# Optimization experiments

Measured on AMD Instinct MI355X. Metric: run time of the kernel, lower is better.

Reference implementation:

```python
import jax, jax.numpy as jnp
import numpy as np
import math

D_MODEL = 1024
N_HEADS = 16
DH = D_MODEL // N_HEADS
THETA = 10000.0


def _rope_tables(S):
    # freqs: (dh/2,)
    inv_freq = 1.0 / (THETA ** (jnp.arange(0, DH, 2, dtype=jnp.float32) / DH))
    ang = jnp.arange(S, dtype=jnp.float32)[:, None] * inv_freq[None, :]  # (S, dh/2)
    cos = jnp.concatenate([jnp.cos(ang), jnp.cos(ang)], axis=-1)  # (S, dh)
    sin = jnp.concatenate([jnp.sin(ang), jnp.sin(ang)], axis=-1)
    return cos, sin


def _apply_rope(x, cos, sin):
    # x: (B, S, H, dh); rotate-half RoPE
    x1, x2 = jnp.split(x, 2, axis=-1)
    rot = jnp.concatenate([-x2, x1], axis=-1)
    c = cos[None, :, None, :]
    s = sin[None, :, None, :]
    return x * c + rot * s


def setup_inputs() -> dict:
    key = jax.random.key(0)
    k1, k2, k3 = jax.random.split(key, 3)
    x = jax.random.normal(k1, (4, 2048, D_MODEL), dtype=jnp.float32)
    qkv = 0.01 * jax.random.normal(k2, (3 * D_MODEL, D_MODEL), dtype=jnp.float32)
    wo = 0.01 * jax.random.normal(k3, (D_MODEL, D_MODEL), dtype=jnp.float32)
    return {"x": x, "qkv": qkv, "wo": wo}


def reference(x, qkv, wo):
    B, S, D = x.shape
    QKV = x @ qkv.T  # (B, S, 3D)
    Q, K, V = jnp.split(QKV, 3, axis=-1)
    q = Q.reshape(B, S, N_HEADS, DH)
    k = K.reshape(B, S, N_HEADS, DH)
    v = V.reshape(B, S, N_HEADS, DH)
    cos, sin = _rope_tables(S)
    q = _apply_rope(q, cos, sin)
    k = _apply_rope(k, cos, sin)
    # (B, H, S, dh)
    q = q.transpose(0, 2, 1, 3)
    k = k.transpose(0, 2, 1, 3)
    v = v.transpose(0, 2, 1, 3)
    scores = jnp.einsum("bhsd,bhtd->bhst", q, k) / math.sqrt(float(DH))
    mask = jnp.tril(jnp.ones((S, S), dtype=scores.dtype))
    scores = scores * mask
    # faithful to original: any exact-zero entry (masked or incidental) -> -inf
    scores = jnp.where(scores == 0.0, -jnp.inf, scores)
    attn = jax.nn.softmax(scores, axis=-1)
    out = jnp.einsum("bhst,bhtd->bhsd", attn, v)  # (B, H, S, dh)
    out = out.transpose(0, 2, 1, 3).reshape(B, S, D)
    return out @ wo.T
```

## Files before the change

kernel.cpp:

```cpp
#include <hip/hip_runtime.h>
#include <math.h>

typedef __bf16 bf16x8 __attribute__((ext_vector_type(8)));
typedef __bf16 bf16x4 __attribute__((ext_vector_type(4)));
typedef float  floatx4 __attribute__((ext_vector_type(4)));
typedef float  floatx2 __attribute__((ext_vector_type(2)));

#define AS1(p) ((__attribute__((address_space(1))) void*)(p))
#define AS3(p) ((__attribute__((address_space(3))) void*)(p))

#define MASKV (-1.0e30f)
#define SOFTMAX_SCALE_LOG2 0.1803368801111244f
#define ROPE_LOG2F 0.4152410118609203f

#define BARRIER do { __builtin_amdgcn_sched_barrier(0); \
                     __builtin_amdgcn_s_barrier(); \
                     __builtin_amdgcn_sched_barrier(0); } while (0)

__global__ __launch_bounds__(256)
void cvt3_kernel(const float* __restrict__ x, const float* __restrict__ qkv,
                 const float* __restrict__ wo, __bf16* __restrict__ xb,
                 __bf16* __restrict__ qkvb, __bf16* __restrict__ wob,
                 float* __restrict__ rt)
{
    const int bi = blockIdx.x;
    if (bi >= 12288) {
        const int e0 = (bi - 12288) * 1024 + threadIdx.x * 4;
#pragma unroll
        for (int j = 0; j < 4; ++j) {
            const int e = e0 + j;
            const int s = e >> 5, d = e & 31;
            const float f = exp2f(-(float)d * ROPE_LOG2F);
            float sn, cs;
            sincosf((float)s * f, &sn, &cs);
            floatx2 t; t[0] = cs; t[1] = sn;
            *(floatx2*)(rt + e * 2) = t;
        }
        return;
    }
    const float* src;
    __bf16* dst;
    int base;
    if (bi < 8192)       { src = x;   dst = xb;   base = bi * 1024; }
    else if (bi < 11264) { src = qkv; dst = qkvb; base = (bi - 8192) * 1024; }
    else                 { src = wo;  dst = wob;  base = (bi - 11264) * 1024; }

    const int i = base + threadIdx.x * 4;
    const floatx4 v = *(const floatx4*)(src + i);
    bf16x4 o;
    o[0] = (__bf16)v[0]; o[1] = (__bf16)v[1];
    o[2] = (__bf16)v[2]; o[3] = (__bf16)v[3];
    *(bf16x4*)(dst + i) = o;
}

__device__ __forceinline__ void gemm_pipe(const __bf16* __restrict__ Ap,
                                          const __bf16* __restrict__ Bp,
                                          const int m0, const int n0,
                                          __bf16* smem, floatx4 (&acc)[4][4])
{
    const int tid  = threadIdx.x;
    const int wave = tid >> 6;
    const int lane = tid & 63;
    const int quad = lane >> 4;
    const int l16  = lane & 15;
    const int wr   = wave >> 2;
    const int wc   = wave & 3;

    const int arow = wr * 32 + l16;
    const int brow = (wc & 1) * 64 + l16;
    const int bsel = (wc >> 1) * 8192;
    const int swz  = (l16 & 7) << 4;
    int coff[2];
    coff[0] = (( (quad << 4))        ^ swz) >> 1;
    coff[1] = ((64 | (quad << 4))    ^ swz) >> 1;

    auto stageA = [&](int buf, int h, int k0) {
        const int o = tid << 4;
        const int r = o >> 7;
        const int c = (o & 127) ^ ((r & 7) << 4);
        const __bf16* src = Ap + (size_t)(m0 + h * 64 + r) * 1024 + k0 + (c >> 1);
        __builtin_amdgcn_global_load_lds(AS1(src),
            AS3(smem + buf * 24576 + h * 4096 + wave * 512), 16, 0, 0);
    };
    auto stageB = [&](int buf, int h, int k0) {
#pragma unroll
        for (int q = 0; q < 2; ++q) {
            const int o = (q * 512 + tid) << 4;
            const int r = o >> 7;
            const int c = (o & 127) ^ ((r & 7) << 4);
            const __bf16* src = Bp + (size_t)(n0 + h * 128 + r) * 1024 + k0 + (c >> 1);
            __builtin_amdgcn_global_load_lds(AS1(src),
                AS3(smem + buf * 24576 + 8192 + h * 8192 + (q * 8 + wave) * 512), 16, 0, 0);
        }
    };

#define RDA(P, qm, fm, ks) (*(const bf16x8*)(smem + (P) * 24576 + (qm) * 4096 \
                             + ((arow + (fm) * 16) << 6) + coff[ks]))
#define RDB(P, g, ks)      (*(const bf16x8*)(smem + (P) * 24576 + 8192 + bsel \
                             + ((brow + (g) * 16) << 6) + coff[ks]))
#define MFMA8(MB, NB, AV, BV) do { \
    _Pragma("unroll") for (int fm_ = 0; fm_ < 2; ++fm_) \
    _Pragma("unroll") for (int gi_ = 0; gi_ < 2; ++gi_) \
    _Pragma("unroll") for (int ks_ = 0; ks_ < 2; ++ks_) \
        acc[(MB) + fm_][(NB) + gi_] = __builtin_amdgcn_mfma_f32_16x16x32_bf16( \
            AV[fm_][ks_], BV[gi_][ks_], acc[(MB) + fm_][(NB) + gi_], 0, 0, 0); \
} while (0)

    stageA(0, 0, 0);  stageB(0, 0, 0);  stageA(0, 1, 0);  stageB(0, 1, 0);
    stageA(1, 0, 64); stageB(1, 0, 64); stageA(1, 1, 64);
    asm volatile("s_waitcnt vmcnt(4)" ::: "memory");
    BARRIER;

    bf16x8 a0[2][2], a1[2][2], b0[2][2], b1[2][2];

#define TILE(JT, P) do { \
    const int kn_ = ((JT) + 2) * 64; \
     \
    _Pragma("unroll") for (int f_ = 0; f_ < 2; ++f_) \
    _Pragma("unroll") for (int k_ = 0; k_ < 2; ++k_) a0[f_][k_] = RDA(P, 0, f_, k_); \
    _Pragma("unroll") for (int g_ = 0; g_ < 2; ++g_) \
    _Pragma("unroll") for (int k_ = 0; k_ < 2; ++k_) b0[g_][k_] = RDB(P, g_, k_); \
    if ((JT) + 1 < 16) stageB(1 - (P), 1, ((JT) + 1) * 64); \
    BARRIER; \
    __builtin_amdgcn_s_setprio(1); MFMA8(0, 0, a0, b0); __builtin_amdgcn_s_setprio(0); \
    BARRIER; \
     \
    _Pragma("unroll") for (int g_ = 0; g_ < 2; ++g_) \
    _Pragma("unroll") for (int k_ = 0; k_ < 2; ++k_) b1[g_][k_] = RDB(P, 2 + g_, k_); \
    if ((JT) + 2 < 16) stageA(P, 0, kn_); \
    BARRIER; \
    __builtin_amdgcn_s_setprio(1); MFMA8(0, 2, a0, b1); __builtin_amdgcn_s_setprio(0); \
    BARRIER; \
     \
    _Pragma("unroll") for (int f_ = 0; f_ < 2; ++f_) \
    _Pragma("unroll") for (int k_ = 0; k_ < 2; ++k_) a1[f_][k_] = RDA(P, 1, f_, k_); \
    if ((JT) + 2 < 16) stageB(P, 0, kn_); \
    BARRIER; \
    __builtin_amdgcn_s_setprio(1); MFMA8(2, 2, a1, b1); __builtin_amdgcn_s_setprio(0); \
    BARRIER; \
     \
    if ((JT) + 2 < 16) stageA(P, 1, kn_); \
    BARRIER; \
    __builtin_amdgcn_s_setprio(1); MFMA8(2, 0, a1, b0); __builtin_amdgcn_s_setprio(0); \
     \
    if ((JT) + 2 < 16)      { asm volatile("s_waitcnt vmcnt(4)" ::: "memory"); } \
    else if ((JT) + 1 < 16) { asm volatile("s_waitcnt vmcnt(0)" ::: "memory"); } \
    BARRIER; \
} while (0)

    for (int it = 0; it < 8; ++it) {
        TILE(2 * it, 0);
        TILE(2 * it + 1, 1);
    }
#undef TILE
#undef RDA
#undef RDB
#undef MFMA8
}

__global__ __launch_bounds__(512, 2)
void gemm_rope_kernel(const __bf16* __restrict__ A, const __bf16* __restrict__ BT,
                      __bf16* __restrict__ Qr, __bf16* __restrict__ Kr,
                      __bf16* __restrict__ Vt, const float* __restrict__ rt)
{
    extern __shared__ __align__(16) __bf16 smem[];
    const int id  = blockIdx.x;
    const int xcd = id & 7, lid = id >> 3;
    const int tm  = xcd * 8 + lid / 12;
    const int tn  = lid % 12;
    const int m0  = tm * 128, n0 = tn * 256;

    floatx4 acc[4][4] = {};
    gemm_pipe(A, BT, m0, n0, smem, acc);

    const int tid  = threadIdx.x;
    const int wave = tid >> 6;
    const int lane = tid & 63;
    const int quad = lane >> 4, l16 = lane & 15;
    const int wr   = wave >> 2, wc = wave & 3;

    const int gn0    = n0 + wc * 64;
    const int region = gn0 >> 10;
    const int h      = (gn0 >> 6) & 15;

    if (region == 2) {
#pragma unroll
        for (int f = 0; f < 4; ++f) {
            const int gm = m0 + (f >> 1) * 64 + wr * 32 + (f & 1) * 16 + quad * 4;
            const int b = gm >> 11, s = gm & 2047;
#pragma unroll
            for (int g = 0; g < 4; ++g) {
                const int d = g * 16 + l16;
                bf16x4 w;
#pragma unroll
                for (int r = 0; r < 4; ++r) w[r] = (__bf16)acc[f][g][r];
                *(bf16x4*)(Vt + ((size_t)(b * 16 + h) * 64 + d) * 2048 + s) = w;
            }
        }
    } else {
        __bf16* dst = region ? Kr : Qr;
#pragma unroll
        for (int g = 0; g < 2; ++g) {
            const int d1 = g * 16 + l16;
#pragma unroll
            for (int f = 0; f < 4; ++f) {
                const int gm0 = m0 + (f >> 1) * 64 + wr * 32 + (f & 1) * 16 + quad * 4;
                const int b = gm0 >> 11, s0 = gm0 & 2047;
#pragma unroll
                for (int r = 0; r < 4; ++r) {
                    const floatx2 t = *(const floatx2*)(rt + ((s0 + r) * 32 + d1) * 2);
                    const float a1 = acc[f][g][r];
                    const float a2 = acc[f][g + 2][r];
                    __bf16* row = dst + ((size_t)((b * 16 + h) * 2048 + s0 + r)) * 64;
                    row[d1]      = (__bf16)(a1 * t[0] - a2 * t[1]);
                    row[d1 + 32] = (__bf16)(a2 * t[0] + a1 * t[1]);
                }
            }
        }
    }
}

__global__ __launch_bounds__(512, 2)
void gemm_bt_kernel(const __bf16* __restrict__ A, const __bf16* __restrict__ BT,
                    float* __restrict__ C)
{
    extern __shared__ __align__(16) __bf16 smem[];
    const int id  = blockIdx.x;
    const int xcd = id & 7, lid = id >> 3;
    const int tm  = xcd * 8 + (lid >> 2);
    const int tn  = lid & 3;
    const int m0  = tm * 128, n0 = tn * 256;

    floatx4 acc[4][4] = {};
    gemm_pipe(A, BT, m0, n0, smem, acc);

    const int tid  = threadIdx.x;
    const int wave = tid >> 6, lane = tid & 63;
    const int quad = lane >> 4, l16 = lane & 15;
    const int wr   = wave >> 2, wc = wave & 3;

#pragma unroll
    for (int f = 0; f < 4; ++f) {
        const int row = m0 + (f >> 1) * 64 + wr * 32 + (f & 1) * 16 + quad * 4;
#pragma unroll
        for (int g = 0; g < 4; ++g) {
            const int col = n0 + wc * 64 + g * 16 + l16;
#pragma unroll
            for (int r = 0; r < 4; ++r)
                C[(size_t)(row + r) * 1024 + col] = acc[f][g][r];
        }
    }
}

__global__ __launch_bounds__(256, 4)
void attn_kernel(const __bf16* __restrict__ Qr, const __bf16* __restrict__ Kr,
                 const __bf16* __restrict__ Vt, __bf16* __restrict__ ctx)
{
    __shared__ __align__(16) __bf16 Ks[64 * 64];
    __shared__ __align__(16) __bf16 Vs[64 * 64];
    __shared__ __align__(16) __bf16 plds[4][16 * 72];

    const int bh   = blockIdx.x;
    const int b    = bh >> 4, h = bh & 15;
    const int tid  = threadIdx.x;
    const int wave = tid >> 6;
    const int lane = tid & 63;
    const int quad = lane >> 4, l16 = lane & 15;
    const int sw   = l16 & 7;

    const __bf16* Qb = Qr + (size_t)bh * 2048 * 64;
    const __bf16* Kb = Kr + (size_t)bh * 2048 * 64;
    const __bf16* Vb = Vt + (size_t)bh * 64 * 2048;
    __bf16* Pw = &plds[wave][0];

    const int c0   = tid;
    const int row0 = c0 >> 3, jg0 = (c0 & 7) ^ (row0 & 7);
    const int c1   = 256 + tid;
    const int row1 = c1 >> 3, jg1 = (c1 & 7) ^ (row1 & 7);

    const int tiles[2] = { (int)blockIdx.y, 31 - (int)blockIdx.y };

    for (int pass = 0; pass < 2; ++pass) {
        const int q0b  = tiles[pass] * 64;
        const int q0   = q0b + wave * 16;
        const int qa   = q0 + l16;
        const int kend = q0b + 64;

        bf16x8 bq[2];
#pragma unroll
        for (int t = 0; t < 2; ++t)
            bq[t] = *(const bf16x8*)(Qb + (q0 + l16) * 64 + t * 32 + quad * 8);

        floatx4 o[4] = {};
        float lpart = 0.f;

        for (int kt = 0; kt < kend; kt += 64) {
            __builtin_amdgcn_global_load_lds(AS1(Kb + (size_t)(kt + row0) * 64 + jg0 * 8),
                                             AS3(Ks + wave * 512), 16, 0, 0);
            __builtin_amdgcn_global_load_lds(AS1(Vb + (size_t)row0 * 2048 + kt + jg0 * 8),
                                             AS3(Vs + wave * 512), 16, 0, 0);
            __builtin_amdgcn_global_load_lds(AS1(Kb + (size_t)(kt + row1) * 64 + jg1 * 8),
                                             AS3(Ks + (4 + wave) * 512), 16, 0, 0);
            __builtin_amdgcn_global_load_lds(AS1(Vb + (size_t)row1 * 2048 + kt + jg1 * 8),
                                             AS3(Vs + (4 + wave) * 512), 16, 0, 0);
            asm volatile("s_waitcnt vmcnt(0)" ::: "memory");
            __syncthreads();

            floatx4 s[4] = {};
#pragma unroll
            for (int st = 0; st < 4; ++st) {
                bf16x8 ka0 = *(const bf16x8*)(Ks + (st * 16 + l16) * 64 + ((0 + quad) ^ sw) * 8);
                bf16x8 ka1 = *(const bf16x8*)(Ks + (st * 16 + l16) * 64 + ((4 + quad) ^ sw) * 8);
                s[st] = __builtin_amdgcn_mfma_f32_16x16x32_bf16(ka0, bq[0], s[st], 0, 0, 0);
                s[st] = __builtin_amdgcn_mfma_f32_16x16x32_bf16(ka1, bq[1], s[st], 0, 0, 0);
            }

#pragma unroll
            for (int st = 0; st < 4; ++st) {
                bf16x4 w;
#pragma unroll
                for (int r = 0; r < 4; ++r) {
                    const int key = kt + st * 16 + quad * 4 + r;
                    const float v = (key > qa) ? MASKV : s[st][r] * SOFTMAX_SCALE_LOG2;
                    const float p = __builtin_amdgcn_exp2f(v);
                    lpart += p;
                    w[r] = (__bf16)p;
                }
                *(bf16x4*)(Pw + l16 * 72 + st * 16 + quad * 4) = w;
            }

            asm volatile("s_waitcnt lgkmcnt(0)" ::: "memory");
            bf16x8 ap0 = *(const bf16x8*)(Pw + l16 * 72 + quad * 8);
            bf16x8 ap1 = *(const bf16x8*)(Pw + l16 * 72 + 32 + quad * 8);

#pragma unroll
            for (int nt = 0; nt < 4; ++nt) {
                bf16x8 bv0 = *(const bf16x8*)(Vs + (nt * 16 + l16) * 64 + ((0 + quad) ^ sw) * 8);
                bf16x8 bv1 = *(const bf16x8*)(Vs + (nt * 16 + l16) * 64 + ((4 + quad) ^ sw) * 8);
                o[nt] = __builtin_amdgcn_mfma_f32_16x16x32_bf16(ap0, bv0, o[nt], 0, 0, 0);
                o[nt] = __builtin_amdgcn_mfma_f32_16x16x32_bf16(ap1, bv1, o[nt], 0, 0, 0);
            }

            __syncthreads();
        }

        float l = lpart;
        l += __shfl_xor(l, 16, 64);
        l += __shfl_xor(l, 32, 64);
        float lr[4];
#pragma unroll
        for (int r = 0; r < 4; ++r)
            lr[r] = __shfl(l, quad * 4 + r, 64);
#pragma unroll
        for (int nt = 0; nt < 4; ++nt)
#pragma unroll
            for (int r = 0; r < 4; ++r) {
                const int srow = q0 + quad * 4 + r;
                const float inv_l = 1.0f / fmaxf(lr[r], 1e-20f);
                ctx[((size_t)(b * 2048 + srow)) * 1024 + h * 64 + nt * 16 + l16] =
                    (__bf16)(o[nt][r] * inv_l);
            }
    }
}

extern "C" void kernel_launch(void* const* d_in, const int* in_sizes, int n_in,
                              void* d_out, int out_size, void* d_ws, size_t ws_size,
                              hipStream_t stream)
{
    const float* x   = (const float*)d_in[0];
    const float* qkv = (const float*)d_in[1];
    const float* wo  = (const float*)d_in[2];
    float* out = (float*)d_out;

    char* ws = (char*)d_ws;
    const size_t MB = 1024 * 1024;
    __bf16* xb   = (__bf16*)(ws);
    __bf16* qkvb = (__bf16*)(ws + 16 * MB);
    __bf16* wob  = (__bf16*)(ws + 22 * MB);
    __bf16* Qr   = (__bf16*)(ws + 24 * MB);
    __bf16* Kr   = (__bf16*)(ws + 40 * MB);
    __bf16* Vt   = (__bf16*)(ws + 56 * MB);
    __bf16* ctx  = (__bf16*)(ws + 72 * MB);
    float*  rt   = (float*) (ws + 88 * MB);

    hipFuncSetAttribute((const void*)gemm_rope_kernel,
                        hipFuncAttributeMaxDynamicSharedMemorySize, 98304);
    hipFuncSetAttribute((const void*)gemm_bt_kernel,
                        hipFuncAttributeMaxDynamicSharedMemorySize, 98304);

    cvt3_kernel<<<12352, 256, 0, stream>>>(x, qkv, wo, xb, qkvb, wob, rt);
    gemm_rope_kernel<<<768, 512, 98304, stream>>>(xb, qkvb, Qr, Kr, Vt, rt);
    attn_kernel<<<dim3(64, 16), 256, 0, stream>>>(Qr, Kr, Vt, ctx);
    gemm_bt_kernel<<<256, 512, 98304, stream>>>(ctx, wob, out);
}
```

Before: 229.8 us.

## Double-buffer K/V tiles in attention and fold softmax scale into Q

```diff
diff --git a/kernel.cpp b/kernel.cpp
--- a/kernel.cpp
+++ b/kernel.cpp
@@ -115,7 +115,6 @@
 
 #define TILE(JT, P) do { \
     const int kn_ = ((JT) + 2) * 64; \
-     \
     _Pragma("unroll") for (int f_ = 0; f_ < 2; ++f_) \
     _Pragma("unroll") for (int k_ = 0; k_ < 2; ++k_) a0[f_][k_] = RDA(P, 0, f_, k_); \
     _Pragma("unroll") for (int g_ = 0; g_ < 2; ++g_) \
@@ -124,25 +123,21 @@
     BARRIER; \
     __builtin_amdgcn_s_setprio(1); MFMA8(0, 0, a0, b0); __builtin_amdgcn_s_setprio(0); \
     BARRIER; \
-     \
     _Pragma("unroll") for (int g_ = 0; g_ < 2; ++g_) \
     _Pragma("unroll") for (int k_ = 0; k_ < 2; ++k_) b1[g_][k_] = RDB(P, 2 + g_, k_); \
     if ((JT) + 2 < 16) stageA(P, 0, kn_); \
     BARRIER; \
     __builtin_amdgcn_s_setprio(1); MFMA8(0, 2, a0, b1); __builtin_amdgcn_s_setprio(0); \
     BARRIER; \
-     \
     _Pragma("unroll") for (int f_ = 0; f_ < 2; ++f_) \
     _Pragma("unroll") for (int k_ = 0; k_ < 2; ++k_) a1[f_][k_] = RDA(P, 1, f_, k_); \
     if ((JT) + 2 < 16) stageB(P, 0, kn_); \
     BARRIER; \
     __builtin_amdgcn_s_setprio(1); MFMA8(2, 2, a1, b1); __builtin_amdgcn_s_setprio(0); \
     BARRIER; \
-     \
     if ((JT) + 2 < 16) stageA(P, 1, kn_); \
     BARRIER; \
     __builtin_amdgcn_s_setprio(1); MFMA8(2, 0, a1, b0); __builtin_amdgcn_s_setprio(0); \
-     \
     if ((JT) + 2 < 16)      { asm volatile("s_waitcnt vmcnt(4)" ::: "memory"); } \
     else if ((JT) + 1 < 16) { asm volatile("s_waitcnt vmcnt(0)" ::: "memory"); } \
     BARRIER; \
@@ -199,6 +194,7 @@
         }
     } else {
         __bf16* dst = region ? Kr : Qr;
+        const float sc = region ? 1.0f : SOFTMAX_SCALE_LOG2;
 #pragma unroll
         for (int g = 0; g < 2; ++g) {
             const int d1 = g * 16 + l16;
@@ -212,8 +208,8 @@
                     const float a1 = acc[f][g][r];
                     const float a2 = acc[f][g + 2][r];
                     __bf16* row = dst + ((size_t)((b * 16 + h) * 2048 + s0 + r)) * 64;
-                    row[d1]      = (__bf16)(a1 * t[0] - a2 * t[1]);
-                    row[d1 + 32] = (__bf16)(a2 * t[0] + a1 * t[1]);
+                    row[d1]      = (__bf16)((a1 * t[0] - a2 * t[1]) * sc);
+                    row[d1 + 32] = (__bf16)((a2 * t[0] + a1 * t[1]) * sc);
                 }
             }
         }
@@ -252,12 +248,12 @@
     }
 }
 
-__global__ __launch_bounds__(256, 4)
+__global__ __launch_bounds__(256, 3)
 void attn_kernel(const __bf16* __restrict__ Qr, const __bf16* __restrict__ Kr,
                  const __bf16* __restrict__ Vt, __bf16* __restrict__ ctx)
 {
-    __shared__ __align__(16) __bf16 Ks[64 * 64];
-    __shared__ __align__(16) __bf16 Vs[64 * 64];
+    __shared__ __align__(16) __bf16 Ks[2][64 * 64];
+    __shared__ __align__(16) __bf16 Vs[2][64 * 64];
     __shared__ __align__(16) __bf16 plds[4][16 * 72];
 
     const int bh   = blockIdx.x;
@@ -280,11 +276,22 @@
 
     const int tiles[2] = { (int)blockIdx.y, 31 - (int)blockIdx.y };
 
+    auto stage = [&](int buf, int kt) {
+        __builtin_amdgcn_global_load_lds(AS1(Kb + (size_t)(kt + row0) * 64 + jg0 * 8),
+                                         AS3(&Ks[buf][0] + wave * 512), 16, 0, 0);
+        __builtin_amdgcn_global_load_lds(AS1(Vb + (size_t)row0 * 2048 + kt + jg0 * 8),
+                                         AS3(&Vs[buf][0] + wave * 512), 16, 0, 0);
+        __builtin_amdgcn_global_load_lds(AS1(Kb + (size_t)(kt + row1) * 64 + jg1 * 8),
+                                         AS3(&Ks[buf][0] + (4 + wave) * 512), 16, 0, 0);
+        __builtin_amdgcn_global_load_lds(AS1(Vb + (size_t)row1 * 2048 + kt + jg1 * 8),
+                                         AS3(&Vs[buf][0] + (4 + wave) * 512), 16, 0, 0);
+    };
+
     for (int pass = 0; pass < 2; ++pass) {
-        const int q0b  = tiles[pass] * 64;
-        const int q0   = q0b + wave * 16;
-        const int qa   = q0 + l16;
-        const int kend = q0b + 64;
+        const int q0b   = tiles[pass] * 64;
+        const int q0    = q0b + wave * 16;
+        const int qa    = q0 + l16;
+        const int ntile = tiles[pass] + 1;
 
         bf16x8 bq[2];
 #pragma unroll
@@ -294,55 +301,56 @@
         floatx4 o[4] = {};
         float lpart = 0.f;
 
-        for (int kt = 0; kt < kend; kt += 64) {
-            __builtin_amdgcn_global_load_lds(AS1(Kb + (size_t)(kt + row0) * 64 + jg0 * 8),
-                                             AS3(Ks + wave * 512), 16, 0, 0);
-            __builtin_amdgcn_global_load_lds(AS1(Vb + (size_t)row0 * 2048 + kt + jg0 * 8),
-                                             AS3(Vs + wave * 512), 16, 0, 0);
-            __builtin_amdgcn_global_load_lds(AS1(Kb + (size_t)(kt + row1) * 64 + jg1 * 8),
-                                             AS3(Ks + (4 + wave) * 512), 16, 0, 0);
-            __builtin_amdgcn_global_load_lds(AS1(Vb + (size_t)row1 * 2048 + kt + jg1 * 8),
-                                             AS3(Vs + (4 + wave) * 512), 16, 0, 0);
-            asm volatile("s_waitcnt vmcnt(0)" ::: "memory");
-            __syncthreads();
-
-            floatx4 s[4] = {};
-#pragma unroll
-            for (int st = 0; st < 4; ++st) {
-                bf16x8 ka0 = *(const bf16x8*)(Ks + (st * 16 + l16) * 64 + ((0 + quad) ^ sw) * 8);
-                bf16x8 ka1 = *(const bf16x8*)(Ks + (st * 16 + l16) * 64 + ((4 + quad) ^ sw) * 8);
-                s[st] = __builtin_amdgcn_mfma_f32_16x16x32_bf16(ka0, bq[0], s[st], 0, 0, 0);
-                s[st] = __builtin_amdgcn_mfma_f32_16x16x32_bf16(ka1, bq[1], s[st], 0, 0, 0);
-            }
-
-#pragma unroll
-            for (int st = 0; st < 4; ++st) {
-                bf16x4 w;
-#pragma unroll
-                for (int r = 0; r < 4; ++r) {
-                    const int key = kt + st * 16 + quad * 4 + r;
-                    const float v = (key > qa) ? MASKV : s[st][r] * SOFTMAX_SCALE_LOG2;
-                    const float p = __builtin_amdgcn_exp2f(v);
-                    lpart += p;
-                    w[r] = (__bf16)p;
-                }
-                *(bf16x4*)(Pw + l16 * 72 + st * 16 + quad * 4) = w;
-            }
-
-            asm volatile("s_waitcnt lgkmcnt(0)" ::: "memory");
-            bf16x8 ap0 = *(const bf16x8*)(Pw + l16 * 72 + quad * 8);
-            bf16x8 ap1 = *(const bf16x8*)(Pw + l16 * 72 + 32 + quad * 8);
-
-#pragma unroll
-            for (int nt = 0; nt < 4; ++nt) {
-                bf16x8 bv0 = *(const bf16x8*)(Vs + (nt * 16 + l16) * 64 + ((0 + quad) ^ sw) * 8);
-                bf16x8 bv1 = *(const bf16x8*)(Vs + (nt * 16 + l16) * 64 + ((4 + quad) ^ sw) * 8);
-                o[nt] = __builtin_amdgcn_mfma_f32_16x16x32_bf16(ap0, bv0, o[nt], 0, 0, 0);
-                o[nt] = __builtin_amdgcn_mfma_f32_16x16x32_bf16(ap1, bv1, o[nt], 0, 0, 0);
-            }
-
-            __syncthreads();
-        }
+        __syncthreads();
+        stage(0, 0);
+
+#define ATT_TILE(CUR, KT, MASKED, HASNEXT) do {                                   \
+    asm volatile("s_waitcnt vmcnt(0)" ::: "memory");                              \
+    BARRIER;                                                                      \
+    const __bf16* Kc = &Ks[CUR][0];                                               \
+    const __bf16* Vc = &Vs[CUR][0];                                               \
+    floatx4 s[4] = {};                                                            \
+    __builtin_amdgcn_s_setprio(1);                                                \
+    _Pragma("unroll") for (int st = 0; st < 4; ++st) {                            \
+        bf16x8 ka0 = *(const bf16x8*)(Kc + (st * 16 + l16) * 64 + ((0 + quad) ^ sw) * 8); \
+        bf16x8 ka1 = *(const bf16x8*)(Kc + (st * 16 + l16) * 64 + ((4 + quad) ^ sw) * 8); \
+        s[st] = __builtin_amdgcn_mfma_f32_16x16x32_bf16(ka0, bq[0], s[st], 0, 0, 0); \
+        s[st] = __builtin_amdgcn_mfma_f32_16x16x32_bf16(ka1, bq[1], s[st], 0, 0, 0); \
+    }                                                                             \
+    __builtin_amdgcn_s_setprio(0);                                                \
+    if (HASNEXT) stage(1 - (CUR), (KT) + 64);                                     \
+    _Pragma("unroll") for (int st = 0; st < 4; ++st) {                            \
+        bf16x4 w;                                                                 \
+        _Pragma("unroll") for (int r = 0; r < 4; ++r) {                           \
+            float v = s[st][r];                                                   \
+            if (MASKED) {                                                         \
+                const int key = (KT) + st * 16 + quad * 4 + r;                    \
+                v = (key > qa) ? MASKV : v;                                       \
+            }                                                                     \
+            const float p = __builtin_amdgcn_exp2f(v);                            \
+            lpart += p;                                                           \
+            w[r] = (__bf16)p;                                                     \
+        }                                                                         \
+        *(bf16x4*)(Pw + l16 * 72 + st * 16 + quad * 4) = w;                       \
+    }                                                                             \
+    asm volatile("s_waitcnt lgkmcnt(0)" ::: "memory");                            \
+    bf16x8 ap0 = *(const bf16x8*)(Pw + l16 * 72 + quad * 8);                      \
+    bf16x8 ap1 = *(const bf16x8*)(Pw + l16 * 72 + 32 + quad * 8);                 \
+    __builtin_amdgcn_s_setprio(1);                                                \
+    _Pragma("unroll") for (int n2 = 0; n2 < 4; ++n2) {                            \
+        bf16x8 bv0 = *(const bf16x8*)(Vc + (n2 * 16 + l16) * 64 + ((0 + quad) ^ sw) * 8); \
+        bf16x8 bv1 = *(const bf16x8*)(Vc + (n2 * 16 + l16) * 64 + ((4 + quad) ^ sw) * 8); \
+        o[n2] = __builtin_amdgcn_mfma_f32_16x16x32_bf16(ap0, bv0, o[n2], 0, 0, 0); \
+        o[n2] = __builtin_amdgcn_mfma_f32_16x16x32_bf16(ap1, bv1, o[n2], 0, 0, 0); \
+    }                                                                             \
+    __builtin_amdgcn_s_setprio(0);                                                \
+} while (0)
+
+        for (int t = 0; t < ntile - 1; ++t)
+            ATT_TILE(t & 1, t * 64, 0, 1);
+        ATT_TILE((ntile - 1) & 1, (ntile - 1) * 64, 1, 0);
+
+#undef ATT_TILE
 
         float l = lpart;
         l += __shfl_xor(l, 16, 64);
```

Measured after the change: 250.7 us. +9.1%, slower.

## Widen attention blocks to 128 queries and fold softmax scale into Q

Applied to the files above, without the earlier changes.

```diff
diff --git a/kernel.cpp b/kernel.cpp
--- a/kernel.cpp
+++ b/kernel.cpp
@@ -115,7 +115,6 @@
 
 #define TILE(JT, P) do { \
     const int kn_ = ((JT) + 2) * 64; \
-     \
     _Pragma("unroll") for (int f_ = 0; f_ < 2; ++f_) \
     _Pragma("unroll") for (int k_ = 0; k_ < 2; ++k_) a0[f_][k_] = RDA(P, 0, f_, k_); \
     _Pragma("unroll") for (int g_ = 0; g_ < 2; ++g_) \
@@ -124,25 +123,21 @@
     BARRIER; \
     __builtin_amdgcn_s_setprio(1); MFMA8(0, 0, a0, b0); __builtin_amdgcn_s_setprio(0); \
     BARRIER; \
-     \
     _Pragma("unroll") for (int g_ = 0; g_ < 2; ++g_) \
     _Pragma("unroll") for (int k_ = 0; k_ < 2; ++k_) b1[g_][k_] = RDB(P, 2 + g_, k_); \
     if ((JT) + 2 < 16) stageA(P, 0, kn_); \
     BARRIER; \
     __builtin_amdgcn_s_setprio(1); MFMA8(0, 2, a0, b1); __builtin_amdgcn_s_setprio(0); \
     BARRIER; \
-     \
     _Pragma("unroll") for (int f_ = 0; f_ < 2; ++f_) \
     _Pragma("unroll") for (int k_ = 0; k_ < 2; ++k_) a1[f_][k_] = RDA(P, 1, f_, k_); \
     if ((JT) + 2 < 16) stageB(P, 0, kn_); \
     BARRIER; \
     __builtin_amdgcn_s_setprio(1); MFMA8(2, 2, a1, b1); __builtin_amdgcn_s_setprio(0); \
     BARRIER; \
-     \
     if ((JT) + 2 < 16) stageA(P, 1, kn_); \
     BARRIER; \
     __builtin_amdgcn_s_setprio(1); MFMA8(2, 0, a1, b0); __builtin_amdgcn_s_setprio(0); \
-     \
     if ((JT) + 2 < 16)      { asm volatile("s_waitcnt vmcnt(4)" ::: "memory"); } \
     else if ((JT) + 1 < 16) { asm volatile("s_waitcnt vmcnt(0)" ::: "memory"); } \
     BARRIER; \
@@ -199,6 +194,7 @@
         }
     } else {
         __bf16* dst = region ? Kr : Qr;
+        const float sc = region ? 1.0f : SOFTMAX_SCALE_LOG2;
 #pragma unroll
         for (int g = 0; g < 2; ++g) {
             const int d1 = g * 16 + l16;
@@ -212,8 +208,8 @@
                     const float a1 = acc[f][g][r];
                     const float a2 = acc[f][g + 2][r];
                     __bf16* row = dst + ((size_t)((b * 16 + h) * 2048 + s0 + r)) * 64;
-                    row[d1]      = (__bf16)(a1 * t[0] - a2 * t[1]);
-                    row[d1 + 32] = (__bf16)(a2 * t[0] + a1 * t[1]);
+                    row[d1]      = (__bf16)((a1 * t[0] - a2 * t[1]) * sc);
+                    row[d1 + 32] = (__bf16)((a2 * t[0] + a1 * t[1]) * sc);
                 }
             }
         }
@@ -252,13 +248,13 @@
     }
 }
 
-__global__ __launch_bounds__(256, 4)
+__global__ __launch_bounds__(512, 8)
 void attn_kernel(const __bf16* __restrict__ Qr, const __bf16* __restrict__ Kr,
                  const __bf16* __restrict__ Vt, __bf16* __restrict__ ctx)
 {
     __shared__ __align__(16) __bf16 Ks[64 * 64];
     __shared__ __align__(16) __bf16 Vs[64 * 64];
-    __shared__ __align__(16) __bf16 plds[4][16 * 72];
+    __shared__ __align__(16) __bf16 plds[8][16 * 72];
 
     const int bh   = blockIdx.x;
     const int b    = bh >> 4, h = bh & 15;
@@ -273,18 +269,17 @@
     const __bf16* Vb = Vt + (size_t)bh * 64 * 2048;
     __bf16* Pw = &plds[wave][0];
 
-    const int c0   = tid;
-    const int row0 = c0 >> 3, jg0 = (c0 & 7) ^ (row0 & 7);
-    const int c1   = 256 + tid;
-    const int row1 = c1 >> 3, jg1 = (c1 & 7) ^ (row1 & 7);
-
-    const int tiles[2] = { (int)blockIdx.y, 31 - (int)blockIdx.y };
+    const int row0 = tid >> 3;
+    const int jg0  = (tid & 7) ^ (row0 & 7);
+
+    const int tiles[2] = { (int)blockIdx.y, 15 - (int)blockIdx.y };
 
     for (int pass = 0; pass < 2; ++pass) {
-        const int q0b  = tiles[pass] * 64;
-        const int q0   = q0b + wave * 16;
-        const int qa   = q0 + l16;
-        const int kend = q0b + 64;
+        const int tq    = tiles[pass];
+        const int q0b   = tq * 128;
+        const int q0    = q0b + wave * 16;
+        const int qa    = q0 + l16;
+        const int ntile = 2 * tq + 2;
 
         bf16x8 bq[2];
 #pragma unroll
@@ -294,51 +289,59 @@
         floatx4 o[4] = {};
         float lpart = 0.f;
 
-        for (int kt = 0; kt < kend; kt += 64) {
+        for (int t = 0; t < ntile; ++t) {
+            const int kt = t * 64;
             __builtin_amdgcn_global_load_lds(AS1(Kb + (size_t)(kt + row0) * 64 + jg0 * 8),
                                              AS3(Ks + wave * 512), 16, 0, 0);
             __builtin_amdgcn_global_load_lds(AS1(Vb + (size_t)row0 * 2048 + kt + jg0 * 8),
                                              AS3(Vs + wave * 512), 16, 0, 0);
-            __builtin_amdgcn_global_load_lds(AS1(Kb + (size_t)(kt + row1) * 64 + jg1 * 8),
-                                             AS3(Ks + (4 + wave) * 512), 16, 0, 0);
-            __builtin_amdgcn_global_load_lds(AS1(Vb + (size_t)row1 * 2048 + kt + jg1 * 8),
-                                             AS3(Vs + (4 + wave) * 512), 16, 0, 0);
             asm volatile("s_waitcnt vmcnt(0)" ::: "memory");
             __syncthreads();
 
-            floatx4 s[4] = {};
-#pragma unroll
-            for (int st = 0; st < 4; ++st) {
-                bf16x8 ka0 = *(const bf16x8*)(Ks + (st * 16 + l16) * 64 + ((0 + quad) ^ sw) * 8);
-                bf16x8 ka1 = *(const bf16x8*)(Ks + (st * 16 + l16) * 64 + ((4 + quad) ^ sw) * 8);
-                s[st] = __builtin_amdgcn_mfma_f32_16x16x32_bf16(ka0, bq[0], s[st], 0, 0, 0);
-                s[st] = __builtin_amdgcn_mfma_f32_16x16x32_bf16(ka1, bq[1], s[st], 0, 0, 0);
-            }
-
-#pragma unroll
-            for (int st = 0; st < 4; ++st) {
-                bf16x4 w;
-#pragma unroll
-                for (int r = 0; r < 4; ++r) {
-                    const int key = kt + st * 16 + quad * 4 + r;
-                    const float v = (key > qa) ? MASKV : s[st][r] * SOFTMAX_SCALE_LOG2;
-                    const float p = __builtin_amdgcn_exp2f(v);
-                    lpart += p;
-                    w[r] = (__bf16)p;
+            if (kt <= q0 + 15) {
+                const bool masked = (t >= ntile - 2);
+
+                floatx4 s[4] = {};
+                __builtin_amdgcn_s_setprio(1);
+#pragma unroll
+                for (int st = 0; st < 4; ++st) {
+                    bf16x8 ka0 = *(const bf16x8*)(Ks + (st * 16 + l16) * 64 + ((0 + quad) ^ sw) * 8);
+                    bf16x8 ka1 = *(const bf16x8*)(Ks + (st * 16 + l16) * 64 + ((4 + quad) ^ sw) * 8);
+                    s[st] = __builtin_amdgcn_mfma_f32_16x16x32_bf16(ka0, bq[0], s[st], 0, 0, 0);
+                    s[st] = __builtin_amdgcn_mfma_f32_16x16x32_bf16(ka1, bq[1], s[st], 0, 0, 0);
                 }
-                *(bf16x4*)(Pw + l16 * 72 + st * 16 + quad * 4) = w;
-            }
-
-            asm volatile("s_waitcnt lgkmcnt(0)" ::: "memory");
-            bf16x8 ap0 = *(const bf16x8*)(Pw + l16 * 72 + quad * 8);
-            bf16x8 ap1 = *(const bf16x8*)(Pw + l16 * 72 + 32 + quad * 8);
-
-#pragma unroll
-            for (int nt = 0; nt < 4; ++nt) {
-                bf16x8 bv0 = *(const bf16x8*)(Vs + (nt * 16 + l16) * 64 + ((0 + quad) ^ sw) * 8);
-                bf16x8 bv1 = *(const bf16x8*)(Vs + (nt * 16 + l16) * 64 + ((4 + quad) ^ sw) * 8);
-                o[nt] = __builtin_amdgcn_mfma_f32_16x16x32_bf16(ap0, bv0, o[nt], 0, 0, 0);
-                o[nt] = __builtin_amdgcn_mfma_f32_16x16x32_bf16(ap1, bv1, o[nt], 0, 0, 0);
+                __builtin_amdgcn_s_setprio(0);
+
+#pragma unroll
+                for (int st = 0; st < 4; ++st) {
+                    bf16x4 w;
+#pragma unroll
+                    for (int r = 0; r < 4; ++r) {
+                        float v = s[st][r];
+                        if (masked) {
+                            const int key = kt + st * 16 + quad * 4 + r;
+                            v = (key > qa) ? MASKV : v;
+                        }
+                        const float p = __builtin_amdgcn_exp2f(v);
+                        lpart += p;
+                        w[r] = (__bf16)p;
+                    }
+                    *(bf16x4*)(Pw + l16 * 72 + st * 16 + quad * 4) = w;
+                }
+
+                asm volatile("s_waitcnt lgkmcnt(0)" ::: "memory");
+                bf16x8 ap0 = *(const bf16x8*)(Pw + l16 * 72 + quad * 8);
+                bf16x8 ap1 = *(const bf16x8*)(Pw + l16 * 72 + 32 + quad * 8);
+
+                __builtin_amdgcn_s_setprio(1);
+#pragma unroll
+                for (int nt = 0; nt < 4; ++nt) {
+                    bf16x8 bv0 = *(const bf16x8*)(Vs + (nt * 16 + l16) * 64 + ((0 + quad) ^ sw) * 8);
+                    bf16x8 bv1 = *(const bf16x8*)(Vs + (nt * 16 + l16) * 64 + ((4 + quad) ^ sw) * 8);
+                    o[nt] = __builtin_amdgcn_mfma_f32_16x16x32_bf16(ap0, bv0, o[nt], 0, 0, 0);
+                    o[nt] = __builtin_amdgcn_mfma_f32_16x16x32_bf16(ap1, bv1, o[nt], 0, 0, 0);
+                }
+                __builtin_amdgcn_s_setprio(0);
             }
 
             __syncthreads();
@@ -390,6 +393,6 @@
 
     cvt3_kernel<<<12352, 256, 0, stream>>>(x, qkv, wo, xb, qkvb, wob, rt);
     gemm_rope_kernel<<<768, 512, 98304, stream>>>(xb, qkvb, Qr, Kr, Vt, rt);
-    attn_kernel<<<dim3(64, 16), 256, 0, stream>>>(Qr, Kr, Vt, ctx);
+    attn_kernel<<<dim3(64, 8), 512, 0, stream>>>(Qr, Kr, Vt, ctx);
     gemm_bt_kernel<<<256, 512, 98304, stream>>>(ctx, wob, out);
 }
```

New measurement: 253.6 us. +10.3%, slower.
